# Optimization experiments

Measured on AMD Instinct MI355X. Metric: run time of the kernel, lower is better.

Reference implementation:

```python
import jax, jax.numpy as jnp
import numpy as np

SEED_THR = 0.5
DUP_THR = 0.8


def _connected_labels(adj):
    """Min-label propagation with pointer jumping; adj: [N,N] bool (diag set for active nodes)."""
    N = adj.shape[0]

    def cond(carry):
        _, changed = carry
        return changed

    def body(carry):
        labels, _ = carry
        nbr_min = jnp.min(jnp.where(adj, labels[None, :], N), axis=1)
        new = jnp.minimum(labels, nbr_min)
        new = jnp.minimum(new, new[new])  # pointer jumping -> O(log N) convergence
        return new, jnp.any(new != labels)

    labels0 = jnp.arange(N)
    labels, _ = jax.lax.while_loop(cond, body, (labels0, jnp.array(True)))
    return labels


def _per_image(sig, scores):
    # sig: [N,C], scores: [N]
    N = sig.shape[0]
    idx = jnp.arange(N)
    sel = scores >= SEED_THR
    # fallback: if nothing passes the threshold, select argmax score
    sel = jnp.where(sel.any(), sel, idx == jnp.argmax(scores))

    # cosine pairwise similarity
    sn = sig * jax.lax.rsqrt(jnp.sum(sig * sig, axis=-1, keepdims=True) + 1e-12)
    sim = sn @ sn.T  # [N,N]

    adj = (sim >= DUP_THR) & sel[:, None] & sel[None, :]
    adj = adj | jnp.diag(sel)  # diagonal True for selected nodes

    labels = _connected_labels(adj)  # component root = min node index in component

    neg_inf = jnp.float32(-1e30)
    masked_scores = jnp.where(sel, scores, neg_inf)
    comp_max = jnp.full((N,), neg_inf, dtype=scores.dtype).at[labels].max(masked_scores)
    is_best = sel & (scores >= comp_max[labels])
    # tie-break: smallest index (matches torch argmax-first semantics)
    comp_best = jnp.full((N,), N, dtype=jnp.int32).at[labels].min(
        jnp.where(is_best, idx, N).astype(jnp.int32))
    is_seed = sel & (idx == comp_best[labels])

    # compact seeds to the front, ordered by component root (== DFS discovery order)
    sort_key = jnp.where(is_seed, labels, N)
    order = jnp.argsort(sort_key)
    mask = is_seed[order]  # [N] bool, True for valid seed slots
    seed_sig = jnp.where(mask[:, None], sig[order], jnp.zeros((), sig.dtype))
    seed_sc = jnp.where(mask, scores[order], jnp.zeros((), scores.dtype))
    return seed_sig, mask, seed_sc


def reference(query_signatures, query_seed_logits):
    L, B, Q, C = query_signatures.shape
    sig = jnp.transpose(query_signatures, (1, 0, 2, 3)).reshape(B, L * Q, C)
    logits = jnp.transpose(query_seed_logits, (1, 0, 2)).reshape(B, L * Q).astype(jnp.float32)
    scores = jax.nn.sigmoid(logits)
    seed_signatures, pad_mask, seed_scores = jax.vmap(_per_image)(sig, scores)
    return seed_signatures, pad_mask, seed_scores


def setup_inputs() -> dict:
    key = jax.random.key(0)
    k1, k2 = jax.random.split(key)
    L, B, Q, C = 6, 4, 900, 256
    return {
        "query_signatures": jax.random.normal(k1, (L, B, Q, C), dtype=jnp.float32),
        "query_seed_logits": jax.random.normal(k2, (L, B, Q), dtype=jnp.float32),
    }
```

## Files before the change

### kernel.cpp

```cpp
#include <hip/hip_runtime.h>
#include <cstdint>
#include <cstddef>

#define LDIM 6
#define BDIM 4
#define QDIM 900
#define CDIM 256
#define NDIM (LDIM*QDIM)
#define NN   5408
#define T128 43
#define NT128 (T128*(T128+1)/2)

typedef float floatx4 __attribute__((ext_vector_type(4)));

__device__ __forceinline__ int sig_off(int b, int n) {
    int l = n / QDIM, q = n - l * QDIM;
    return ((l * BDIM + b) * QDIM + q) * CDIM;
}
__device__ __forceinline__ int logit_off(int b, int n) {
    int l = n / QDIM, q = n - l * QDIM;
    return (l * BDIM + b) * QDIM + q;
}

__device__ __forceinline__ int uf_load(const int* p, int i) {
    return __hip_atomic_load(&p[i], __ATOMIC_RELAXED, __HIP_MEMORY_SCOPE_AGENT);
}
__device__ int uf_find(int* p, int x) {
    int r = x;
    int pr = uf_load(p, r);
    while (pr != r) { r = pr; pr = uf_load(p, r); }
    return r;
}
__device__ void uf_union(int* p, int a, int b) {
    int ra = uf_find(p, a), rb = uf_find(p, b);
    while (ra != rb) {
        int hi = ra > rb ? ra : rb;
        int lo = ra ^ rb ^ hi;
        int old = atomicCAS(&p[hi], hi, lo);
        if (old == hi) return;
        ra = uf_find(p, old);
        rb = uf_find(p, lo);
    }
}

__device__ __forceinline__ int pk_fp8x4(float a, float b, float c, float d) {
    int p = __builtin_amdgcn_cvt_pk_fp8_f32(a, b, 0, false);
    p = __builtin_amdgcn_cvt_pk_fp8_f32(c, d, p, true);
    return p;
}

__global__ void k_init(const float* __restrict__ logits, float* __restrict__ scores,
                       int* __restrict__ parent, unsigned long long* __restrict__ compKey,
                       int* __restrict__ selIdx, int* __restrict__ Mcnt,
                       unsigned long long* __restrict__ argKey, int* __restrict__ done) {
    int b = blockIdx.y;
    int n = blockIdx.x * 256 + threadIdx.x;
    int lane = threadIdx.x & 63;
    if (n < NN) compKey[b * NN + n] = 0ULL;
    unsigned long long key = 0ULL;
    int f = 0;
    if (n < NDIM) {
        float x = logits[logit_off(b, n)];
        float sc = 1.0f / (1.0f + expf(-x));
        scores[b * NN + n] = sc;
        parent[b * NN + n] = n;
        f = (sc >= 0.5f) ? 1 : 0;
        key = ((unsigned long long)__float_as_uint(sc) << 32) | (unsigned int)(~n);
    }
    unsigned long long bal = __ballot(f != 0);
    int cnt = __popcll(bal);
    int rank = __popcll(bal & ((1ull << lane) - 1ull));
    int base = 0;
    if (lane == 0 && cnt) base = atomicAdd(&Mcnt[b], cnt);
    base = __shfl(base, 0);
    if (f) selIdx[b * NN + base + rank] = n;
    for (int off = 32; off; off >>= 1) {
        unsigned long long o = __shfl_down(key, off);
        if (o > key) key = o;
    }
    if (lane == 0) atomicMax(&argKey[b], key);
    __syncthreads();
    if (threadIdx.x == 0) {
        int prev = __hip_atomic_fetch_add(&done[b], 1, __ATOMIC_ACQ_REL,
                                          __HIP_MEMORY_SCOPE_AGENT);
        if (prev == (int)gridDim.x - 1) {
            if (__hip_atomic_load(&Mcnt[b], __ATOMIC_RELAXED, __HIP_MEMORY_SCOPE_AGENT) == 0) {
                unsigned long long k = __hip_atomic_load(&argKey[b], __ATOMIC_RELAXED,
                                                         __HIP_MEMORY_SCOPE_AGENT);
                selIdx[b * NN + 0] = (int)(~(unsigned int)(k & 0xffffffffULL));
                __hip_atomic_store(&Mcnt[b], 1, __ATOMIC_RELAXED, __HIP_MEMORY_SCOPE_AGENT);
            }
        }
    }
}

__global__ void k_tobf(const float* __restrict__ sig, const int* __restrict__ selIdx,
                       const int* __restrict__ Mcnt, char* __restrict__ Xf8) {
    int b = blockIdx.y;
    int g = (blockIdx.x * blockDim.x + threadIdx.x) >> 6;
    int lane = threadIdx.x & 63;
    if (g >= Mcnt[b]) return;
    int node = selIdx[b * NN + g];
    const float4 v = *(const float4*)(sig + sig_off(b, node) + lane * 4);
    float s = v.x * v.x + v.y * v.y + v.z * v.z + v.w * v.w;
    for (int off = 32; off; off >>= 1) s += __shfl_down(s, off);
    s = __shfl(s, 0);
    float ninv = rsqrtf(s + 1e-12f);
    int p = pk_fp8x4(v.x * ninv, v.y * ninv, v.z * ninv, v.w * ninv);
    int slot = (lane >> 2) ^ (g & 15);
    *(int*)(Xf8 + ((size_t)(b * NN + g)) * 256 + slot * 16 + (lane & 3) * 4) = p;
}

__global__ __launch_bounds__(256) void k_sim_mfma(const char* __restrict__ Xf8,
                                                  const int* __restrict__ selIdx,
                                                  const int* __restrict__ Mcnt,
                                                  int* __restrict__ parent) {
    int bx = blockIdx.x;
    int b = bx & 3;
    int t = bx >> 2;
    int M = Mcnt[b];
    int ti = (int)((sqrtf(8.0f * (float)t + 1.0f) - 1.0f) * 0.5f);
    while ((ti + 1) * (ti + 2) / 2 <= t) ti++;
    while (ti * (ti + 1) / 2 > t) ti--;
    int tj = t - ti * (ti + 1) / 2;
    if (ti * 128 >= M) return;

    extern __shared__ char Bs[];

    int tid = threadIdx.x;
    int lane = tid & 63, wave = tid >> 6;
    int rsel = lane & 15, quad = lane >> 4;

    const char* xb = Xf8 + ((size_t)b * NN) * 256;
#pragma unroll
    for (int k = 0; k < 8; k++) {
        int i = wave * 8 + k;
        int row = min(tj * 128 + 4 * i, NN - 4);
        const char* src = xb + (size_t)row * 256 + lane * 16;
        __builtin_amdgcn_global_load_lds(
            (const __attribute__((address_space(1))) unsigned int*)src,
            (__attribute__((address_space(3))) unsigned int*)(Bs + i * 1024),
            16, 0, 0);
    }

    int rA = ti * 128 + wave * 32;
    int gA0 = min(rA + rsel, M - 1);
    int gA1 = min(rA + 16 + rsel, M - 1);
    const char* pA0 = Xf8 + ((size_t)(b * NN + gA0)) * 256;
    const char* pA1 = Xf8 + ((size_t)(b * NN + gA1)) * 256;
    int swA0 = gA0 & 15, swA1 = gA1 & 15;

    __syncthreads();

    floatx4 acc[2][8];
#pragma unroll
    for (int s = 0; s < 2; s++)
#pragma unroll
        for (int nj = 0; nj < 8; nj++) acc[s][nj] = (floatx4){0.f, 0.f, 0.f, 0.f};

#pragma unroll
    for (int ks = 0; ks < 8; ks++) {
        int ch = ks * 2 + (quad >> 1);
        int ih = (quad & 1) * 8;
        long a0 = *(const long*)(pA0 + ((ch ^ swA0) << 4) + ih);
        long a1 = *(const long*)(pA1 + ((ch ^ swA1) << 4) + ih);
#pragma unroll
        for (int nj = 0; nj < 8; nj++) {
            int lr = nj * 16 + rsel;
            long bb = *(const long*)(Bs + lr * 256 + (((ch ^ (lr & 15)) << 4) + ih));
            acc[0][nj] = __builtin_amdgcn_mfma_f32_16x16x32_fp8_fp8(a0, bb, acc[0][nj], 0, 0, 0);
            acc[1][nj] = __builtin_amdgcn_mfma_f32_16x16x32_fp8_fp8(a1, bb, acc[1][nj], 0, 0, 0);
        }
    }

#pragma unroll
    for (int s = 0; s < 2; s++) {
        int rowA = rA + s * 16 + quad * 4;
#pragma unroll
        for (int nj = 0; nj < 8; nj++) {
            int gj = tj * 128 + nj * 16 + rsel;
#pragma unroll
            for (int r = 0; r < 4; r++) {
                int gi = rowA + r;
                if (gi < M && gj < M && gi > gj && acc[s][nj][r] >= 0.8f) {
                    uf_union(parent + b * NN, selIdx[b * NN + gi], selIdx[b * NN + gj]);
                }
            }
        }
    }
}

__global__ __launch_bounds__(1024) void k_comp(int* __restrict__ parent,
                                               const int* __restrict__ selIdx,
                                               const int* __restrict__ Mcnt,
                                               const float* __restrict__ scores,
                                               unsigned long long* __restrict__ compKey,
                                               int* __restrict__ seedNode,
                                               int* __restrict__ Scnt) {
    int b = blockIdx.x, t = threadIdx.x;
    int lane = t & 63, w = t >> 6;
    __shared__ int wsum[16];
    __shared__ int sbase;
    if (t == 0) sbase = 0;
    __syncthreads();

    int M = Mcnt[b];
    for (int base = 0; base < M; base += 1024) {
        int g = base + t;
        if (g < M) {
            int node = selIdx[b * NN + g];
            int root = uf_find(parent + b * NN, node);
            unsigned long long key =
                ((unsigned long long)__float_as_uint(scores[b * NN + node]) << 32) |
                (unsigned int)(~node);
            atomicMax(&compKey[b * NN + root], key);
        }
    }
    __syncthreads();

    for (int base = 0; base < NDIM; base += 1024) {
        int n = base + t;
        unsigned long long key = 0ULL;
        if (n < NDIM)
            key = __hip_atomic_load(&compKey[b * NN + n], __ATOMIC_RELAXED,
                                    __HIP_MEMORY_SCOPE_AGENT);
        int f = (key != 0ULL) ? 1 : 0;
        unsigned long long bal = __ballot(f != 0);
        int rank = __popcll(bal & ((1ull << lane) - 1ull));
        if (lane == 0) wsum[w] = __popcll(bal);
        __syncthreads();
        if (t == 0) {
            int s = sbase;
            for (int i = 0; i < 16; i++) { int v = wsum[i]; wsum[i] = s; s += v; }
            sbase = s;
        }
        __syncthreads();
        if (f) seedNode[b * NN + wsum[w] + rank] = (int)(~(unsigned int)(key & 0xffffffffULL));
        __syncthreads();
    }
    if (t == 0) Scnt[b] = sbase;
}

__global__ void k_write(const float* __restrict__ sig, const float* __restrict__ scores,
                        const int* __restrict__ seedNode, const int* __restrict__ Scnt,
                        float* __restrict__ out) {
    int b = blockIdx.y;
    int slot = blockIdx.x * 4 + (threadIdx.x >> 6);
    int lane = threadIdx.x & 63;
    float* orow = out + ((size_t)(b * NDIM + slot)) * CDIM + lane * 4;
    if (slot < Scnt[b]) {
        int s = seedNode[b * NN + slot];
        float4 v = *(const float4*)(sig + sig_off(b, s) + lane * 4);
        *(float4*)orow = v;
        if (lane == 0) {
            out[(size_t)BDIM * NDIM * CDIM + (size_t)b * NDIM + slot] = 1.0f;
            out[(size_t)BDIM * NDIM * CDIM + (size_t)BDIM * NDIM + (size_t)b * NDIM + slot] =
                scores[b * NN + s];
        }
    } else {
        float4 z = {0.f, 0.f, 0.f, 0.f};
        *(float4*)orow = z;
        if (lane == 0) {
            out[(size_t)BDIM * NDIM * CDIM + (size_t)b * NDIM + slot] = 0.0f;
            out[(size_t)BDIM * NDIM * CDIM + (size_t)BDIM * NDIM + (size_t)b * NDIM + slot] = 0.0f;
        }
    }
}

extern "C" void kernel_launch(void* const* d_in, const int* in_sizes, int n_in,
                              void* d_out, int out_size, void* d_ws, size_t ws_size,
                              hipStream_t stream) {
    (void)in_sizes; (void)n_in; (void)out_size; (void)ws_size;
    const float* sig = (const float*)d_in[0];
    const float* logits = (const float*)d_in[1];
    float* out = (float*)d_out;
    char* ws = (char*)d_ws;

    const size_t arr = (size_t)BDIM * NN * 4;
    int* Mcnt = (int*)(ws + 0);
    int* Scnt = (int*)(ws + 64);
    unsigned long long* argKey = (unsigned long long*)(ws + 128);
    int* done = (int*)(ws + 192);
    unsigned long long* compKey = (unsigned long long*)(ws + 256);
    float* scores = (float*)(ws + 256 + 2 * arr);
    int* parent   = (int*)(ws + 256 + 3 * arr);
    int* selIdx   = (int*)(ws + 256 + 4 * arr);
    int* seedNode = (int*)(ws + 256 + 5 * arr);
    char* Xf8     = (char*)(ws + 256 + 6 * arr);

    hipMemsetAsync(ws, 0, 512, stream);

    k_init<<<dim3((NN + 255) / 256, BDIM), 256, 0, stream>>>(
        logits, scores, parent, compKey, selIdx, Mcnt, argKey, done);
    k_tobf<<<dim3((NDIM + 3) / 4, BDIM), 256, 0, stream>>>(sig, selIdx, Mcnt, Xf8);
    k_sim_mfma<<<NT128 * BDIM, 256, 32768, stream>>>(Xf8, selIdx, Mcnt, parent);
    k_comp<<<BDIM, 1024, 0, stream>>>(parent, selIdx, Mcnt, scores, compKey, seedNode, Scnt);
    k_write<<<dim3(NDIM / 4, BDIM), 256, 0, stream>>>(sig, scores, seedNode, Scnt, out);
}
```

Baseline: 110.5 us.

## Fuse init with fp8 conversion and fold component reduction into similarity kernel

Merges the score/selection kernel with the fp8 normalisation kernel, so each block converts its own selected rows and the last block per image handles the argmax fallback. The component-max and seed-compaction pass moves into the tail of the similarity kernel through a last-block-done counter, and it uses a two-pass per-wave count instead of the old per-chunk block scans. This removes two kernel launches and their gaps. In exchange, the final compaction runs in a single 256-thread block per image, and the fallback path rewrites row 0 after other blocks may already have written it.

```diff
diff --git a/kernel.cpp b/kernel.cpp
--- a/kernel.cpp
+++ b/kernel.cpp
@@ -49,72 +49,120 @@
     return p;
 }
 
-__global__ void k_init(const float* __restrict__ logits, float* __restrict__ scores,
-                       int* __restrict__ parent, unsigned long long* __restrict__ compKey,
-                       int* __restrict__ selIdx, int* __restrict__ Mcnt,
-                       unsigned long long* __restrict__ argKey, int* __restrict__ done) {
+__global__ __launch_bounds__(1024) void k_prep(const float* __restrict__ logits,
+                                               const float* __restrict__ sig,
+                                               float* __restrict__ scores,
+                                               int* __restrict__ parent,
+                                               unsigned long long* __restrict__ compKey,
+                                               int* __restrict__ selIdx,
+                                               int* __restrict__ Mcnt,
+                                               char* __restrict__ Xf8,
+                                               int* __restrict__ doneP) {
     int b = blockIdx.y;
-    int n = blockIdx.x * 256 + threadIdx.x;
-    int lane = threadIdx.x & 63;
-    if (n < NN) compKey[b * NN + n] = 0ULL;
+    int t = threadIdx.x;
+    int lane = t & 63, wv = t >> 6;
+    __shared__ int selNodeSh[64];
+    __shared__ int cntSh, baseSh;
+    int blockBase = blockIdx.x * 64;
+
+    if (wv == 0) {
+        int n = blockBase + lane;
+        int f = 0;
+        if (n < NDIM) {
+            float x = logits[logit_off(b, n)];
+            float sc = 1.0f / (1.0f + expf(-x));
+            scores[b * NN + n] = sc;
+            parent[b * NN + n] = n;
+            compKey[b * NN + n] = 0ULL;
+            f = (sc >= 0.5f) ? 1 : 0;
+        }
+        unsigned long long bal = __ballot(f != 0);
+        int cnt = __popcll(bal);
+        int rank = __popcll(bal & ((1ull << lane) - 1ull));
+        int base = 0;
+        if (lane == 0 && cnt) base = atomicAdd(&Mcnt[b], cnt);
+        if (lane == 0) { cntSh = cnt; baseSh = base; }
+        base = __shfl(base, 0);
+        if (f) {
+            selNodeSh[rank] = n;
+            selIdx[b * NN + base + rank] = n;
+        }
+    }
+    __syncthreads();
+
+    int cnt = cntSh, base = baseSh;
+    for (int i = wv; i < cnt; i += 16) {
+        int node = selNodeSh[i];
+        int g = base + i;
+        const float4 v = *(const float4*)(sig + sig_off(b, node) + lane * 4);
+        float s = v.x * v.x + v.y * v.y + v.z * v.z + v.w * v.w;
+        for (int off = 32; off; off >>= 1) s += __shfl_down(s, off);
+        s = __shfl(s, 0);
+        float ninv = rsqrtf(s + 1e-12f);
+        int p = pk_fp8x4(v.x * ninv, v.y * ninv, v.z * ninv, v.w * ninv);
+        int slot = (lane >> 2) ^ (g & 15);
+        *(int*)(Xf8 + ((size_t)(b * NN + g)) * 256 + slot * 16 + (lane & 3) * 4) = p;
+    }
+
+    __syncthreads();
+    __shared__ int lastSh;
+    if (t == 0) {
+        int prev = __hip_atomic_fetch_add(&doneP[b], 1, __ATOMIC_ACQ_REL,
+                                          __HIP_MEMORY_SCOPE_AGENT);
+        lastSh = (prev == (int)gridDim.x - 1) ? 1 : 0;
+    }
+    __syncthreads();
+    if (!lastSh) return;
+    if (__hip_atomic_load(&Mcnt[b], __ATOMIC_RELAXED, __HIP_MEMORY_SCOPE_AGENT) != 0)
+        return;
+
+    __shared__ unsigned long long redSh[16];
+    __shared__ int bestSh;
     unsigned long long key = 0ULL;
-    int f = 0;
-    if (n < NDIM) {
-        float x = logits[logit_off(b, n)];
-        float sc = 1.0f / (1.0f + expf(-x));
-        scores[b * NN + n] = sc;
-        parent[b * NN + n] = n;
-        f = (sc >= 0.5f) ? 1 : 0;
-        key = ((unsigned long long)__float_as_uint(sc) << 32) | (unsigned int)(~n);
-    }
-    unsigned long long bal = __ballot(f != 0);
-    int cnt = __popcll(bal);
-    int rank = __popcll(bal & ((1ull << lane) - 1ull));
-    int base = 0;
-    if (lane == 0 && cnt) base = atomicAdd(&Mcnt[b], cnt);
-    base = __shfl(base, 0);
-    if (f) selIdx[b * NN + base + rank] = n;
+    for (int n = t; n < NDIM; n += 1024) {
+        float sc = __hip_atomic_load(&scores[b * NN + n], __ATOMIC_RELAXED,
+                                     __HIP_MEMORY_SCOPE_AGENT);
+        unsigned long long k2 =
+            ((unsigned long long)__float_as_uint(sc) << 32) | (unsigned int)(~n);
+        if (k2 > key) key = k2;
+    }
     for (int off = 32; off; off >>= 1) {
         unsigned long long o = __shfl_down(key, off);
         if (o > key) key = o;
     }
-    if (lane == 0) atomicMax(&argKey[b], key);
-    __syncthreads();
-    if (threadIdx.x == 0) {
-        int prev = __hip_atomic_fetch_add(&done[b], 1, __ATOMIC_ACQ_REL,
-                                          __HIP_MEMORY_SCOPE_AGENT);
-        if (prev == (int)gridDim.x - 1) {
-            if (__hip_atomic_load(&Mcnt[b], __ATOMIC_RELAXED, __HIP_MEMORY_SCOPE_AGENT) == 0) {
-                unsigned long long k = __hip_atomic_load(&argKey[b], __ATOMIC_RELAXED,
-                                                         __HIP_MEMORY_SCOPE_AGENT);
-                selIdx[b * NN + 0] = (int)(~(unsigned int)(k & 0xffffffffULL));
-                __hip_atomic_store(&Mcnt[b], 1, __ATOMIC_RELAXED, __HIP_MEMORY_SCOPE_AGENT);
-            }
-        }
-    }
-}
-
-__global__ void k_tobf(const float* __restrict__ sig, const int* __restrict__ selIdx,
-                       const int* __restrict__ Mcnt, char* __restrict__ Xf8) {
-    int b = blockIdx.y;
-    int g = (blockIdx.x * blockDim.x + threadIdx.x) >> 6;
-    int lane = threadIdx.x & 63;
-    if (g >= Mcnt[b]) return;
-    int node = selIdx[b * NN + g];
-    const float4 v = *(const float4*)(sig + sig_off(b, node) + lane * 4);
-    float s = v.x * v.x + v.y * v.y + v.z * v.z + v.w * v.w;
-    for (int off = 32; off; off >>= 1) s += __shfl_down(s, off);
-    s = __shfl(s, 0);
-    float ninv = rsqrtf(s + 1e-12f);
-    int p = pk_fp8x4(v.x * ninv, v.y * ninv, v.z * ninv, v.w * ninv);
-    int slot = (lane >> 2) ^ (g & 15);
-    *(int*)(Xf8 + ((size_t)(b * NN + g)) * 256 + slot * 16 + (lane & 3) * 4) = p;
+    if (lane == 0) redSh[wv] = key;
+    __syncthreads();
+    if (t == 0) {
+        unsigned long long kk = redSh[0];
+        for (int i = 1; i < 16; i++) if (redSh[i] > kk) kk = redSh[i];
+        int bestNode = (int)(~(unsigned int)(kk & 0xffffffffULL));
+        selIdx[b * NN + 0] = bestNode;
+        __hip_atomic_store(&Mcnt[b], 1, __ATOMIC_RELAXED, __HIP_MEMORY_SCOPE_AGENT);
+        bestSh = bestNode;
+    }
+    __syncthreads();
+    if (wv == 0) {
+        int node = bestSh;
+        const float4 v = *(const float4*)(sig + sig_off(b, node) + lane * 4);
+        float s = v.x * v.x + v.y * v.y + v.z * v.z + v.w * v.w;
+        for (int off = 32; off; off >>= 1) s += __shfl_down(s, off);
+        s = __shfl(s, 0);
+        float ninv = rsqrtf(s + 1e-12f);
+        int p = pk_fp8x4(v.x * ninv, v.y * ninv, v.z * ninv, v.w * ninv);
+        int slot = (lane >> 2);
+        *(int*)(Xf8 + ((size_t)(b * NN + 0)) * 256 + slot * 16 + (lane & 3) * 4) = p;
+    }
 }
 
 __global__ __launch_bounds__(256) void k_sim_mfma(const char* __restrict__ Xf8,
                                                   const int* __restrict__ selIdx,
                                                   const int* __restrict__ Mcnt,
-                                                  int* __restrict__ parent) {
+                                                  int* __restrict__ parent,
+                                                  const float* __restrict__ scores,
+                                                  unsigned long long* __restrict__ compKey,
+                                                  int* __restrict__ seedNode,
+                                                  int* __restrict__ Scnt,
+                                                  int* __restrict__ doneS) {
     int bx = blockIdx.x;
     int b = bx & 3;
     int t = bx >> 2;
@@ -123,7 +171,7 @@
     while ((ti + 1) * (ti + 2) / 2 <= t) ti++;
     while (ti * (ti + 1) / 2 > t) ti--;
     int tj = t - ti * (ti + 1) / 2;
-    if (ti * 128 >= M) return;
+    int active = (ti * 128 < M);
 
     extern __shared__ char Bs[];
 
@@ -131,114 +179,118 @@
     int lane = tid & 63, wave = tid >> 6;
     int rsel = lane & 15, quad = lane >> 4;
 
-    const char* xb = Xf8 + ((size_t)b * NN) * 256;
-#pragma unroll
-    for (int k = 0; k < 8; k++) {
-        int i = wave * 8 + k;
-        int row = min(tj * 128 + 4 * i, NN - 4);
-        const char* src = xb + (size_t)row * 256 + lane * 16;
-        __builtin_amdgcn_global_load_lds(
-            (const __attribute__((address_space(1))) unsigned int*)src,
-            (__attribute__((address_space(3))) unsigned int*)(Bs + i * 1024),
-            16, 0, 0);
-    }
-
-    int rA = ti * 128 + wave * 32;
-    int gA0 = min(rA + rsel, M - 1);
-    int gA1 = min(rA + 16 + rsel, M - 1);
-    const char* pA0 = Xf8 + ((size_t)(b * NN + gA0)) * 256;
-    const char* pA1 = Xf8 + ((size_t)(b * NN + gA1)) * 256;
-    int swA0 = gA0 & 15, swA1 = gA1 & 15;
-
-    __syncthreads();
-
-    floatx4 acc[2][8];
-#pragma unroll
-    for (int s = 0; s < 2; s++)
-#pragma unroll
-        for (int nj = 0; nj < 8; nj++) acc[s][nj] = (floatx4){0.f, 0.f, 0.f, 0.f};
-
-#pragma unroll
-    for (int ks = 0; ks < 8; ks++) {
-        int ch = ks * 2 + (quad >> 1);
-        int ih = (quad & 1) * 8;
-        long a0 = *(const long*)(pA0 + ((ch ^ swA0) << 4) + ih);
-        long a1 = *(const long*)(pA1 + ((ch ^ swA1) << 4) + ih);
-#pragma unroll
-        for (int nj = 0; nj < 8; nj++) {
-            int lr = nj * 16 + rsel;
-            long bb = *(const long*)(Bs + lr * 256 + (((ch ^ (lr & 15)) << 4) + ih));
-            acc[0][nj] = __builtin_amdgcn_mfma_f32_16x16x32_fp8_fp8(a0, bb, acc[0][nj], 0, 0, 0);
-            acc[1][nj] = __builtin_amdgcn_mfma_f32_16x16x32_fp8_fp8(a1, bb, acc[1][nj], 0, 0, 0);
-        }
-    }
-
-#pragma unroll
-    for (int s = 0; s < 2; s++) {
-        int rowA = rA + s * 16 + quad * 4;
-#pragma unroll
-        for (int nj = 0; nj < 8; nj++) {
-            int gj = tj * 128 + nj * 16 + rsel;
-#pragma unroll
-            for (int r = 0; r < 4; r++) {
-                int gi = rowA + r;
-                if (gi < M && gj < M && gi > gj && acc[s][nj][r] >= 0.8f) {
-                    uf_union(parent + b * NN, selIdx[b * NN + gi], selIdx[b * NN + gj]);
+    if (active) {
+        const char* xb = Xf8 + ((size_t)b * NN) * 256;
+#pragma unroll
+        for (int k = 0; k < 8; k++) {
+            int i = wave * 8 + k;
+            int row = min(tj * 128 + 4 * i, NN - 4);
+            const char* src = xb + (size_t)row * 256 + lane * 16;
+            __builtin_amdgcn_global_load_lds(
+                (const __attribute__((address_space(1))) unsigned int*)src,
+                (__attribute__((address_space(3))) unsigned int*)(Bs + i * 1024),
+                16, 0, 0);
+        }
+
+        int rA = ti * 128 + wave * 32;
+        int gA0 = min(rA + rsel, M - 1);
+        int gA1 = min(rA + 16 + rsel, M - 1);
+        const char* pA0 = Xf8 + ((size_t)(b * NN + gA0)) * 256;
+        const char* pA1 = Xf8 + ((size_t)(b * NN + gA1)) * 256;
+        int swA0 = gA0 & 15, swA1 = gA1 & 15;
+
+        __syncthreads();
+
+        floatx4 acc[2][8];
+#pragma unroll
+        for (int s = 0; s < 2; s++)
+#pragma unroll
+            for (int nj = 0; nj < 8; nj++) acc[s][nj] = (floatx4){0.f, 0.f, 0.f, 0.f};
+
+#pragma unroll
+        for (int ks = 0; ks < 8; ks++) {
+            int ch = ks * 2 + (quad >> 1);
+            int ih = (quad & 1) * 8;
+            long a0 = *(const long*)(pA0 + ((ch ^ swA0) << 4) + ih);
+            long a1 = *(const long*)(pA1 + ((ch ^ swA1) << 4) + ih);
+#pragma unroll
+            for (int nj = 0; nj < 8; nj++) {
+                int lr = nj * 16 + rsel;
+                long bb = *(const long*)(Bs + lr * 256 + (((ch ^ (lr & 15)) << 4) + ih));
+                acc[0][nj] = __builtin_amdgcn_mfma_f32_16x16x32_fp8_fp8(a0, bb, acc[0][nj], 0, 0, 0);
+                acc[1][nj] = __builtin_amdgcn_mfma_f32_16x16x32_fp8_fp8(a1, bb, acc[1][nj], 0, 0, 0);
+            }
+        }
+
+#pragma unroll
+        for (int s = 0; s < 2; s++) {
+            int rowA = rA + s * 16 + quad * 4;
+#pragma unroll
+            for (int nj = 0; nj < 8; nj++) {
+                int gj = tj * 128 + nj * 16 + rsel;
+#pragma unroll
+                for (int r = 0; r < 4; r++) {
+                    int gi = rowA + r;
+                    if (gi < M && gj < M && gi > gj && acc[s][nj][r] >= 0.8f) {
+                        uf_union(parent + b * NN, selIdx[b * NN + gi], selIdx[b * NN + gj]);
+                    }
                 }
             }
         }
     }
-}
-
-__global__ __launch_bounds__(1024) void k_comp(int* __restrict__ parent,
-                                               const int* __restrict__ selIdx,
-                                               const int* __restrict__ Mcnt,
-                                               const float* __restrict__ scores,
-                                               unsigned long long* __restrict__ compKey,
-                                               int* __restrict__ seedNode,
-                                               int* __restrict__ Scnt) {
-    int b = blockIdx.x, t = threadIdx.x;
-    int lane = t & 63, w = t >> 6;
-    __shared__ int wsum[16];
-    __shared__ int sbase;
-    if (t == 0) sbase = 0;
-    __syncthreads();
-
-    int M = Mcnt[b];
-    for (int base = 0; base < M; base += 1024) {
-        int g = base + t;
-        if (g < M) {
-            int node = selIdx[b * NN + g];
-            int root = uf_find(parent + b * NN, node);
-            unsigned long long key =
-                ((unsigned long long)__float_as_uint(scores[b * NN + node]) << 32) |
-                (unsigned int)(~node);
-            atomicMax(&compKey[b * NN + root], key);
-        }
-    }
-    __syncthreads();
-
-    for (int base = 0; base < NDIM; base += 1024) {
-        int n = base + t;
+
+    __shared__ int lastSh;
+    __syncthreads();
+    if (tid == 0) {
+        int prev = __hip_atomic_fetch_add(&doneS[b], 1, __ATOMIC_ACQ_REL,
+                                          __HIP_MEMORY_SCOPE_AGENT);
+        lastSh = (prev == NT128 - 1) ? 1 : 0;
+    }
+    __syncthreads();
+    if (!lastSh) return;
+
+    for (int g = tid; g < M; g += 256) {
+        int node = selIdx[b * NN + g];
+        int root = uf_find(parent + b * NN, node);
+        unsigned long long key =
+            ((unsigned long long)__float_as_uint(scores[b * NN + node]) << 32) |
+            (unsigned int)(~node);
+        atomicMax(&compKey[b * NN + root], key);
+    }
+    __syncthreads();
+
+    __shared__ int wcnt4[4], woff4[4];
+    const int RW = 22;
+    int cnt = 0;
+    for (int r = 0; r < RW; r++) {
+        int n = wave * 1408 + r * 64 + lane;
         unsigned long long key = 0ULL;
         if (n < NDIM)
             key = __hip_atomic_load(&compKey[b * NN + n], __ATOMIC_RELAXED,
                                     __HIP_MEMORY_SCOPE_AGENT);
-        int f = (key != 0ULL) ? 1 : 0;
-        unsigned long long bal = __ballot(f != 0);
+        cnt += __popcll(__ballot(key != 0ULL));
+    }
+    if (lane == 0) wcnt4[wave] = cnt;
+    __syncthreads();
+    if (tid == 0) {
+        int s = 0;
+        for (int i = 0; i < 4; i++) { woff4[i] = s; s += wcnt4[i]; }
+        Scnt[b] = s;
+    }
+    __syncthreads();
+    int off = woff4[wave];
+    for (int r = 0; r < RW; r++) {
+        int n = wave * 1408 + r * 64 + lane;
+        unsigned long long key = 0ULL;
+        if (n < NDIM)
+            key = __hip_atomic_load(&compKey[b * NN + n], __ATOMIC_RELAXED,
+                                    __HIP_MEMORY_SCOPE_AGENT);
+        unsigned long long bal = __ballot(key != 0ULL);
         int rank = __popcll(bal & ((1ull << lane) - 1ull));
-        if (lane == 0) wsum[w] = __popcll(bal);
-        __syncthreads();
-        if (t == 0) {
-            int s = sbase;
-            for (int i = 0; i < 16; i++) { int v = wsum[i]; wsum[i] = s; s += v; }
-            sbase = s;
-        }
-        __syncthreads();
-        if (f) seedNode[b * NN + wsum[w] + rank] = (int)(~(unsigned int)(key & 0xffffffffULL));
-        __syncthreads();
-    }
-    if (t == 0) Scnt[b] = sbase;
+        if (key != 0ULL)
+            seedNode[b * NN + off + rank] = (int)(~(unsigned int)(key & 0xffffffffULL));
+        off += __popcll(bal);
+    }
 }
 
 __global__ void k_write(const float* __restrict__ sig, const float* __restrict__ scores,
@@ -279,8 +331,8 @@
     const size_t arr = (size_t)BDIM * NN * 4;
     int* Mcnt = (int*)(ws + 0);
     int* Scnt = (int*)(ws + 64);
-    unsigned long long* argKey = (unsigned long long*)(ws + 128);
-    int* done = (int*)(ws + 192);
+    int* doneP = (int*)(ws + 128);
+    int* doneS = (int*)(ws + 192);
     unsigned long long* compKey = (unsigned long long*)(ws + 256);
     float* scores = (float*)(ws + 256 + 2 * arr);
     int* parent   = (int*)(ws + 256 + 3 * arr);
@@ -290,10 +342,9 @@
 
     hipMemsetAsync(ws, 0, 512, stream);
 
-    k_init<<<dim3((NN + 255) / 256, BDIM), 256, 0, stream>>>(
-        logits, scores, parent, compKey, selIdx, Mcnt, argKey, done);
-    k_tobf<<<dim3((NDIM + 3) / 4, BDIM), 256, 0, stream>>>(sig, selIdx, Mcnt, Xf8);
-    k_sim_mfma<<<NT128 * BDIM, 256, 32768, stream>>>(Xf8, selIdx, Mcnt, parent);
-    k_comp<<<BDIM, 1024, 0, stream>>>(parent, selIdx, Mcnt, scores, compKey, seedNode, Scnt);
+    k_prep<<<dim3((NDIM + 63) / 64, BDIM), 1024, 0, stream>>>(
+        logits, sig, scores, parent, compKey, selIdx, Mcnt, Xf8, doneP);
+    k_sim_mfma<<<NT128 * BDIM, 256, 32768, stream>>>(
+        Xf8, selIdx, Mcnt, parent, scores, compKey, seedNode, Scnt, doneS);
     k_write<<<dim3(NDIM / 4, BDIM), 256, 0, stream>>>(sig, scores, seedNode, Scnt, out);
 }
```

Result: slower. 200.8 us (+81.7%).
